# Kernel optimization log

Measured on AMD Instinct MI355X. Metric: run time of the kernel, lower is better.

Reference implementation:

```python
import jax, jax.numpy as jnp
import numpy as np

B, N, IN_F, OUT_F, H = 16, 1024, 256, 256, 4
D = OUT_F // H  # head_dim = 64
NEG_SLOPE = 0.2


def setup_inputs() -> dict:
    key = jax.random.key(0)
    k1, k2, k3 = jax.random.split(key, 3)
    h = jax.random.normal(k1, (B, N, IN_F), dtype=jnp.float32)
    mask = jnp.ones((B, N), dtype=jnp.int32)
    W = jax.random.normal(k2, (OUT_F, IN_F), dtype=jnp.float32) * (1.0 / np.sqrt(IN_F))
    a = jax.random.normal(k3, (2 * D, 1), dtype=jnp.float32) * 0.1
    return {"h": h, "mask": mask, "W": W, "a": a}


def reference(h, mask, W, a):
    # Wh = h @ W.T -> (B, N, OUT_F) -> (B, H, N, D)
    Wh = jnp.einsum('bnf,of->bno', h, W)
    Wh = Wh.reshape(h.shape[0], h.shape[1], H, D).transpose(0, 2, 1, 3)
    # Additive split: cat([Wh_i, Wh_j]) @ a == Wh_i @ a1 + Wh_j @ a2 (same math,
    # avoids the O(N^2 * 2D) concat tensor)
    a1 = a[:D, 0]  # (D,)
    a2 = a[D:, 0]  # (D,)
    s1 = jnp.einsum('bhnd,d->bhn', Wh, a1)  # score for node i
    s2 = jnp.einsum('bhnd,d->bhn', Wh, a2)  # score for node j
    e = s1[:, :, :, None] + s2[:, :, None, :]          # (B, H, N, N)
    e = jnp.where(e >= 0, e, NEG_SLOPE * e)            # LeakyReLU(0.2)
    node_mask = mask.astype(bool)                      # (B, N)
    mm = node_mask[:, None, :, None] & node_mask[:, None, None, :]  # (B,1,N,N)
    e = jnp.where(mm, e, -jnp.inf)
    attn = jax.nn.softmax(e, axis=-1)
    # dropout is identity in eval mode
    attn = jnp.where(mm, attn, 0.0)
    h_prime = jnp.einsum('bhij,bhjd->bhid', attn, Wh)  # (B, H, N, D)
    h_prime = h_prime.transpose(0, 2, 1, 3).reshape(h.shape[0], h.shape[1], OUT_F)
    return h_prime * mask.astype(h_prime.dtype)[:, :, None]
```

## Files before the change

kernel.cpp:

```cpp
#include <hip/hip_runtime.h>

typedef short short8 __attribute__((ext_vector_type(8)));
typedef float floatx4 __attribute__((ext_vector_type(4)));
typedef float floatx16 __attribute__((ext_vector_type(16)));
typedef unsigned int u32;

#define NEG_SLOPE 0.2f

__device__ __forceinline__ u32 pk_rtne(float a, float b) {
    u32 ua = __float_as_uint(a); ua += 0x7fffu + ((ua >> 16) & 1u);
    u32 ub = __float_as_uint(b); ub += 0x7fffu + ((ub >> 16) & 1u);
    return __builtin_amdgcn_perm(ub, ua, 0x07060302);
}
__device__ __forceinline__ u32 pk_trunc(float a, float b) {
    return __builtin_amdgcn_perm(__float_as_uint(b), __float_as_uint(a), 0x07060302);
}
__device__ __forceinline__ void gl_lds16(const void* g, void* l) {
    __builtin_amdgcn_global_load_lds((__attribute__((address_space(1))) u32*)(void*)g,
                                     (__attribute__((address_space(3))) u32*)l, 16, 0, 0);
}

__global__ __launch_bounds__(256, 4) void k_wh(
    const float* __restrict__ hin, const int* __restrict__ mask,
    const float* __restrict__ W, const float* __restrict__ a,
    unsigned short* __restrict__ WhF, float2* __restrict__ E1F1,
    float2* __restrict__ E2F2)
{
    __shared__ unsigned short sBF[8 * 4 * 64 * 8];
    __shared__ float sV1[256], sV2[256];

    const int t = threadIdx.x;
    const int bi = blockIdx.x;
    const int mtile = bi & 255, hh = bi >> 8;
    const int m0g = mtile * 64;
    const int b = m0g >> 10, i0 = m0g & 1023;
    const int b4h = b * 4 + hh;
    const int wid = t >> 6, lane = t & 63;
    const int l15 = lane & 15, q = lane >> 4;

    sV1[t] = 0.f;
    sV2[t] = 0.f;
    __syncthreads();

    float vp1[8] = {0, 0, 0, 0, 0, 0, 0, 0};
    float vp2[8] = {0, 0, 0, 0, 0, 0, 0, 0};
    {
        const int c = t & 31;
        const int rb = t >> 5;
#pragma unroll
        for (int i = 0; i < 8; ++i) {
            int row = i * 8 + rb;
            const float* gp = &W[((size_t)(hh * 64 + row)) * 256 + c * 8];
            float4 w0 = *(const float4*)gp;
            float4 w1 = *(const float4*)(gp + 4);
            float a1r = a[row], a2r = a[64 + row];
            vp1[0] += a1r * w0.x; vp1[1] += a1r * w0.y; vp1[2] += a1r * w0.z; vp1[3] += a1r * w0.w;
            vp1[4] += a1r * w1.x; vp1[5] += a1r * w1.y; vp1[6] += a1r * w1.z; vp1[7] += a1r * w1.w;
            vp2[0] += a2r * w0.x; vp2[1] += a2r * w0.y; vp2[2] += a2r * w0.z; vp2[3] += a2r * w0.w;
            vp2[4] += a2r * w1.x; vp2[5] += a2r * w1.y; vp2[6] += a2r * w1.z; vp2[7] += a2r * w1.w;
            uint4 pv;
            pv.x = pk_rtne(w0.x, w0.y); pv.y = pk_rtne(w0.z, w0.w);
            pv.z = pk_rtne(w1.x, w1.y); pv.w = pk_rtne(w1.z, w1.w);
            int kt = c >> 2, qq = c & 3, nt = row >> 4, r15 = row & 15;
            int idx16 = (kt * 4 + nt) * 64 + qq * 16 + r15;
            *(uint4*)&sBF[(idx16 ^ kt) * 8] = pv;
        }
    }
#pragma unroll
    for (int j = 0; j < 8; ++j) {
        vp1[j] += __shfl_xor(vp1[j], 32, 64);
        vp2[j] += __shfl_xor(vp2[j], 32, 64);
    }
    if (lane < 32) {
        const int c = t & 31;
#pragma unroll
        for (int j = 0; j < 8; ++j) {
            atomicAdd(&sV1[c * 8 + j], vp1[j]);
            atomicAdd(&sV2[c * 8 + j], vp2[j]);
        }
    }
    __syncthreads();

    floatx4 acc[4];
#pragma unroll
    for (int nt = 0; nt < 4; ++nt) {
        floatx4 z = {0.f, 0.f, 0.f, 0.f};
        acc[nt] = z;
    }
    float s1a = 0.f, s2a = 0.f;
    const float* hrow = &hin[((size_t)(m0g + wid * 16 + l15)) * 256 + q * 8];
#pragma unroll
    for (int kt = 0; kt < 8; ++kt) {
        float4 h0 = *(const float4*)(hrow + kt * 32);
        float4 h1 = *(const float4*)(hrow + kt * 32 + 4);
        float4 v1a = *(const float4*)&sV1[kt * 32 + q * 8];
        float4 v1b = *(const float4*)&sV1[kt * 32 + q * 8 + 4];
        float4 v2a = *(const float4*)&sV2[kt * 32 + q * 8];
        float4 v2b = *(const float4*)&sV2[kt * 32 + q * 8 + 4];
        s1a += h0.x * v1a.x + h0.y * v1a.y + h0.z * v1a.z + h0.w * v1a.w
             + h1.x * v1b.x + h1.y * v1b.y + h1.z * v1b.z + h1.w * v1b.w;
        s2a += h0.x * v2a.x + h0.y * v2a.y + h0.z * v2a.z + h0.w * v2a.w
             + h1.x * v2b.x + h1.y * v2b.y + h1.z * v2b.z + h1.w * v2b.w;
        union { short8 s; uint4 u; } af;
        af.u.x = pk_rtne(h0.x, h0.y); af.u.y = pk_rtne(h0.z, h0.w);
        af.u.z = pk_rtne(h1.x, h1.y); af.u.w = pk_rtne(h1.z, h1.w);
#pragma unroll
        for (int nt = 0; nt < 4; ++nt) {
            int idx16 = (kt * 4 + nt) * 64 + lane;
            short8 bf = *(const short8*)&sBF[(idx16 ^ kt) * 8];
            acc[nt] = __builtin_amdgcn_mfma_f32_16x16x32_bf16(af.s, bf, acc[nt], 0, 0, 0);
        }
    }

    const int jt16 = (i0 >> 4) + wid;
    const int g = q & 1, jb = (q >> 1) * 4;
#pragma unroll
    for (int nt = 0; nt < 4; ++nt) {
        int nt32 = nt >> 1;
        int l31 = (nt & 1) * 16 + l15;
        uint2 pv;
        pv.x = pk_rtne(acc[nt][0], acc[nt][1]);
        pv.y = pk_rtne(acc[nt][2], acc[nt][3]);
        size_t idx = ((((size_t)b4h * 64 + jt16) * 2 + nt32) * 64 + (g * 32 + l31)) * 8 + jb;
        *(uint2*)&WhF[idx] = pv;
    }

    s1a += __shfl_xor(s1a, 16, 64); s1a += __shfl_xor(s1a, 32, 64);
    s2a += __shfl_xor(s2a, 16, 64); s2a += __shfl_xor(s2a, 32, 64);
    if (lane < 16) {
        int i = i0 + wid * 16 + lane;
        E1F1[(size_t)b4h * 1024 + i] = make_float2(__expf(s1a), __expf(NEG_SLOPE * s1a));
        int mj = mask[b * 1024 + i];
        E2F2[(size_t)b4h * 1024 + i] =
            make_float2(mj ? __expf(s2a) : 0.f, mj ? __expf(NEG_SLOPE * s2a) : 0.f);
    }
}

__global__ __launch_bounds__(256, 2) void k_attn(
    const int* __restrict__ mask,
    const unsigned short* __restrict__ WhF,
    const float2* __restrict__ E1F1, const float2* __restrict__ E2F2,
    float* __restrict__ out)
{
    __shared__ unsigned short sB[2][8192];

    const int t = threadIdx.x;
    const int bi = blockIdx.x;
    const int b4h = bi & 63, ib = bi >> 6;
    const int b = b4h >> 2, hh = b4h & 3;
    const int i0 = ib * 128;
    const int wid = t >> 6, lane = t & 63;
    const int l31 = lane & 31, g = lane >> 5;
    const int iw = i0 + wid * 32;

    float2 e1 = E1F1[(size_t)b4h * 1024 + iw + l31];
    const float E1 = e1.x, F1 = e1.y;

    floatx16 acc0, acc1, accL;
#pragma unroll
    for (int r = 0; r < 16; ++r) { acc0[r] = 0.f; acc1[r] = 0.f; accL[r] = 0.f; }
    const short ob = (short)0x3F80;
    const short8 ones = {ob, ob, ob, ob, ob, ob, ob, ob};

    const char* gbase = (const char*)WhF + (size_t)b4h * 131072;
    const float2* EFb = E2F2 + (size_t)b4h * 1024;

    float4 nA0, nA1, nB0, nB1;
    {
        const float4* p = (const float4*)EFb + (g << 1);
        nA0 = p[0]; nA1 = p[1]; nB0 = p[4]; nB1 = p[5];
    }

    {
#pragma unroll
        for (int i = 0; i < 4; ++i)
            gl_lds16(gbase + wid * 4096 + i * 1024 + lane * 16,
                     (char*)&sB[0][0] + wid * 4096 + i * 1024);
    }

    for (int jt = 0; jt < 8; ++jt) {
        const int buf = jt & 1;
        __syncthreads();
        if (jt < 7) {
            const char* gp = gbase + (size_t)(jt + 1) * 16384;
#pragma unroll
            for (int i = 0; i < 4; ++i)
                gl_lds16(gp + wid * 4096 + i * 1024 + lane * 16,
                         (char*)&sB[buf ^ 1][0] + wid * 4096 + i * 1024);
        }
#pragma unroll
        for (int tl = 0; tl < 8; ++tl) {
            const float4 eA0 = nA0, eA1 = nA1, eB0 = nB0, eB1 = nB1;
            {
                const int cn = (jt * 8 + tl + 1) & 63;
                const float4* p = (const float4*)EFb + (cn << 3) + (g << 1);
                nA0 = p[0]; nA1 = p[1]; nB0 = p[4]; nB1 = p[5];
            }
            float w0 = fmaxf(E1 * eA0.x, F1 * eA0.y);
            float w1 = fmaxf(E1 * eA0.z, F1 * eA0.w);
            float w2 = fmaxf(E1 * eA1.x, F1 * eA1.y);
            float w3 = fmaxf(E1 * eA1.z, F1 * eA1.w);
            float w4 = fmaxf(E1 * eB0.x, F1 * eB0.y);
            float w5 = fmaxf(E1 * eB0.z, F1 * eB0.w);
            float w6 = fmaxf(E1 * eB1.x, F1 * eB1.y);
            float w7 = fmaxf(E1 * eB1.z, F1 * eB1.w);
            union { short8 s; u32 u[4]; } af;
            af.u[0] = pk_trunc(w0, w1);
            af.u[1] = pk_trunc(w2, w3);
            af.u[2] = pk_trunc(w4, w5);
            af.u[3] = pk_trunc(w6, w7);
            short8 bf0 = *(const short8*)&sB[buf][((tl * 2 + 0) * 64 + lane) * 8];
            short8 bf1 = *(const short8*)&sB[buf][((tl * 2 + 1) * 64 + lane) * 8];
            acc0 = __builtin_amdgcn_mfma_f32_32x32x16_bf16(af.s, bf0, acc0, 0, 0, 0);
            acc1 = __builtin_amdgcn_mfma_f32_32x32x16_bf16(af.s, bf1, acc1, 0, 0, 0);
            accL = __builtin_amdgcn_mfma_f32_32x32x16_bf16(af.s, ones, accL, 0, 0, 0);
        }
    }

#pragma unroll
    for (int r = 0; r < 16; ++r) {
        int row = (r & 3) + 8 * (r >> 2) + 4 * g;
        int i = iw + row;
        float l = accL[r];
        int mi = mask[b * 1024 + i];
        float inv = (mi && l > 0.f) ? 1.0f / l : 0.f;
        size_t o = ((size_t)(b * 1024 + i)) * 256 + hh * 64;
        out[o + l31] = acc0[r] * inv;
        out[o + 32 + l31] = acc1[r] * inv;
    }
}

extern "C" void kernel_launch(void* const* d_in, const int* in_sizes, int n_in,
                              void* d_out, int out_size, void* d_ws, size_t ws_size,
                              hipStream_t stream) {
    const float* h = (const float*)d_in[0];
    const int* mask = (const int*)d_in[1];
    const float* W = (const float*)d_in[2];
    const float* a = (const float*)d_in[3];
    float* out = (float*)d_out;

    unsigned short* WhF = (unsigned short*)d_ws;
    float2* E1F1 = (float2*)((char*)d_ws + (size_t)64 * 64 * 2 * 64 * 8 * 2);
    float2* E2F2 = E1F1 + 64 * 1024;

    hipLaunchKernelGGL(k_wh, dim3(1024), dim3(256), 0, stream, h, mask, W, a, WhF, E1F1, E2F2);
    hipLaunchKernelGGL(k_attn, dim3(512), dim3(256), 0, stream, mask, WhF, E1F1, E2F2, out);
}
```

Before: 116.9 us.

## Load Wh B-fragments straight from global into registers, stage E2F2 in LDS

The attention kernel no longer double-buffers the Wh tiles through shared memory with per-tile barriers. Each lane now prefetches its MFMA B-fragments directly from global memory into registers one step ahead. The per-node exp scores (E2F2) are copied once into LDS and read from there. This drops the LDS round trip and the eight barriers, but every wave now fetches Wh from global or L2 itself, which adds redundant global traffic and puts load latency behind a prefetch only one step deep.

```diff
diff --git a/kernel.cpp b/kernel.cpp
--- a/kernel.cpp
+++ b/kernel.cpp
@@ -142,7 +142,7 @@
     const float2* __restrict__ E1F1, const float2* __restrict__ E2F2,
     float* __restrict__ out)
 {
-    __shared__ unsigned short sB[2][8192];
+    __shared__ float2 sEF[1024];
 
     const int t = threadIdx.x;
     const int bi = blockIdx.x;
@@ -153,6 +153,12 @@
     const int l31 = lane & 31, g = lane >> 5;
     const int iw = i0 + wid * 32;
 
+    {
+        const char* src = (const char*)(E2F2 + (size_t)b4h * 1024);
+        gl_lds16(src + t * 16, (char*)sEF + t * 16);
+        gl_lds16(src + 4096 + t * 16, (char*)sEF + 4096 + t * 16);
+    }
+
     float2 e1 = E1F1[(size_t)b4h * 1024 + iw + l31];
     const float E1 = e1.x, F1 = e1.y;
 
@@ -162,59 +168,47 @@
     const short ob = (short)0x3F80;
     const short8 ones = {ob, ob, ob, ob, ob, ob, ob, ob};
 
-    const char* gbase = (const char*)WhF + (size_t)b4h * 131072;
-    const float2* EFb = E2F2 + (size_t)b4h * 1024;
-
+    const char* gbase = (const char*)WhF + (size_t)b4h * 131072 + (size_t)lane * 16;
+
+    __syncthreads();
+
+    short8 nb0 = *(const short8*)(gbase);
+    short8 nb1 = *(const short8*)(gbase + 1024);
     float4 nA0, nA1, nB0, nB1;
     {
-        const float4* p = (const float4*)EFb + (g << 1);
-        nA0 = p[0]; nA1 = p[1]; nB0 = p[4]; nB1 = p[5];
-    }
-
-    {
-#pragma unroll
-        for (int i = 0; i < 4; ++i)
-            gl_lds16(gbase + wid * 4096 + i * 1024 + lane * 16,
-                     (char*)&sB[0][0] + wid * 4096 + i * 1024);
-    }
-
-    for (int jt = 0; jt < 8; ++jt) {
-        const int buf = jt & 1;
-        __syncthreads();
-        if (jt < 7) {
-            const char* gp = gbase + (size_t)(jt + 1) * 16384;
-#pragma unroll
-            for (int i = 0; i < 4; ++i)
-                gl_lds16(gp + wid * 4096 + i * 1024 + lane * 16,
-                         (char*)&sB[buf ^ 1][0] + wid * 4096 + i * 1024);
-        }
-#pragma unroll
-        for (int tl = 0; tl < 8; ++tl) {
-            const float4 eA0 = nA0, eA1 = nA1, eB0 = nB0, eB1 = nB1;
-            {
-                const int cn = (jt * 8 + tl + 1) & 63;
-                const float4* p = (const float4*)EFb + (cn << 3) + (g << 1);
-                nA0 = p[0]; nA1 = p[1]; nB0 = p[4]; nB1 = p[5];
-            }
-            float w0 = fmaxf(E1 * eA0.x, F1 * eA0.y);
-            float w1 = fmaxf(E1 * eA0.z, F1 * eA0.w);
-            float w2 = fmaxf(E1 * eA1.x, F1 * eA1.y);
-            float w3 = fmaxf(E1 * eA1.z, F1 * eA1.w);
-            float w4 = fmaxf(E1 * eB0.x, F1 * eB0.y);
-            float w5 = fmaxf(E1 * eB0.z, F1 * eB0.w);
-            float w6 = fmaxf(E1 * eB1.x, F1 * eB1.y);
-            float w7 = fmaxf(E1 * eB1.z, F1 * eB1.w);
-            union { short8 s; u32 u[4]; } af;
-            af.u[0] = pk_trunc(w0, w1);
-            af.u[1] = pk_trunc(w2, w3);
-            af.u[2] = pk_trunc(w4, w5);
-            af.u[3] = pk_trunc(w6, w7);
-            short8 bf0 = *(const short8*)&sB[buf][((tl * 2 + 0) * 64 + lane) * 8];
-            short8 bf1 = *(const short8*)&sB[buf][((tl * 2 + 1) * 64 + lane) * 8];
-            acc0 = __builtin_amdgcn_mfma_f32_32x32x16_bf16(af.s, bf0, acc0, 0, 0, 0);
-            acc1 = __builtin_amdgcn_mfma_f32_32x32x16_bf16(af.s, bf1, acc1, 0, 0, 0);
-            accL = __builtin_amdgcn_mfma_f32_32x32x16_bf16(af.s, ones, accL, 0, 0, 0);
-        }
+        const float4* pA = (const float4*)&sEF[g * 4];
+        const float4* pB = (const float4*)&sEF[8 + g * 4];
+        nA0 = pA[0]; nA1 = pA[1]; nB0 = pB[0]; nB1 = pB[1];
+    }
+
+#pragma unroll 8
+    for (int c = 0; c < 64; ++c) {
+        const short8 bf0 = nb0, bf1 = nb1;
+        const float4 eA0 = nA0, eA1 = nA1, eB0 = nB0, eB1 = nB1;
+        {
+            const int cn = (c + 1) & 63;
+            nb0 = *(const short8*)(gbase + (size_t)cn * 2048);
+            nb1 = *(const short8*)(gbase + (size_t)cn * 2048 + 1024);
+            const float4* pA = (const float4*)&sEF[cn * 16 + g * 4];
+            const float4* pB = (const float4*)&sEF[cn * 16 + 8 + g * 4];
+            nA0 = pA[0]; nA1 = pA[1]; nB0 = pB[0]; nB1 = pB[1];
+        }
+        float w0 = fmaxf(E1 * eA0.x, F1 * eA0.y);
+        float w1 = fmaxf(E1 * eA0.z, F1 * eA0.w);
+        float w2 = fmaxf(E1 * eA1.x, F1 * eA1.y);
+        float w3 = fmaxf(E1 * eA1.z, F1 * eA1.w);
+        float w4 = fmaxf(E1 * eB0.x, F1 * eB0.y);
+        float w5 = fmaxf(E1 * eB0.z, F1 * eB0.w);
+        float w6 = fmaxf(E1 * eB1.x, F1 * eB1.y);
+        float w7 = fmaxf(E1 * eB1.z, F1 * eB1.w);
+        union { short8 s; u32 u[4]; } af;
+        af.u[0] = pk_trunc(w0, w1);
+        af.u[1] = pk_trunc(w2, w3);
+        af.u[2] = pk_trunc(w4, w5);
+        af.u[3] = pk_trunc(w6, w7);
+        acc0 = __builtin_amdgcn_mfma_f32_32x32x16_bf16(af.s, bf0, acc0, 0, 0, 0);
+        acc1 = __builtin_amdgcn_mfma_f32_32x32x16_bf16(af.s, bf1, acc1, 0, 0, 0);
+        accL = __builtin_amdgcn_mfma_f32_32x32x16_bf16(af.s, ones, accL, 0, 0, 0);
     }
 
 #pragma unroll
```

New measurement: 111.6 us. 1.05x faster.
